# Performance work log

Hardware: AMD Instinct MI355X
Metric: run time of the kernel (lower is better)

The kernel has to match this reference:

```python
import jax, jax.numpy as jnp
import numpy as np

H, DH = 16, 32  # hardcoded by E's shape [16, seq, 32]


def setup_inputs() -> dict:
    key = jax.random.key(0)
    k1, k2 = jax.random.split(key)
    B, S = 2, 2048
    x = jax.random.normal(k1, (B, S, 3 * H * DH), dtype=jnp.float32)
    E = jax.random.normal(k2, (H, S, DH), dtype=jnp.float32) * 0.02  # learned rel-pos table
    return {"x": x, "E": E}


def _skew(rel):
    # Music-Transformer skew trick: rel [B,H,S,S] -> relative-position alignment.
    B, Hh, S, _ = rel.shape
    rel = jnp.pad(rel, ((0, 0), (0, 0), (0, 0), (1, 0)))  # pad left on last dim
    rel = rel.reshape(B, Hh, S + 1, S)[:, :, 1:]
    return rel


def reference(x, E):
    B, S, _ = x.shape
    q, k, v = jnp.split(x, 3, axis=2)

    def heads(t):
        return t.reshape(B, S, H, DH).transpose(0, 2, 1, 3)  # [B,H,S,DH]

    q, k, v = heads(q), heads(k), heads(v)
    present = jnp.stack([k, v], axis=1)  # [B,2,H,S,DH]

    w = jnp.einsum('bhsd,bhtd->bhst', q, k)            # content scores
    rel = _skew(jnp.einsum('bhsd,hmd->bhsm', q, E))    # relative-position scores
    w = (w + rel) * jax.lax.rsqrt(jnp.float32(DH))     # scale AFTER adding rel (as in source)

    i = jnp.arange(S)[:, None]
    j = jnp.arange(S)[None, :]
    b = (i >= j).astype(w.dtype)                       # causal mask (nd == ns)
    w = w * b - jnp.float32(1e10) * (1.0 - b)
    w = jax.nn.softmax(w, axis=-1)

    a = jnp.einsum('bhst,bhtd->bhsd', w, v)
    a = a.transpose(0, 2, 1, 3).reshape(B, S, H * DH)  # merge heads -> [B,S,512]
    return a, present
```

## Files before the change

kernel.cpp:

```cpp
#include <hip/hip_runtime.h>
#include <hip/hip_bf16.h>

#define NH   16
#define DHD  32
#define SEQ  2048
#define NB   2
#define XROW 1536
#define PP   72

typedef unsigned short u16;
typedef __attribute__((ext_vector_type(8))) short bf16x8;
typedef __attribute__((ext_vector_type(4))) float f32x4;

static __device__ __forceinline__ u16 f2b(float f) {
    __hip_bfloat16 h = __float2bfloat16(f);
    return *(u16*)&h;
}

__global__ __launch_bounds__(256)
void prep_all(const float* __restrict__ x, const float* __restrict__ E,
              u16* __restrict__ Kb, u16* __restrict__ Vt, u16* __restrict__ Eb) {
    __shared__ float t[64][33];
    int bid = blockIdx.x;
    int tid = threadIdx.x;
    if (bid < 1024) {
        long o = ((long)bid * 256 + tid) * 8;
        int d = (int)(o & 31);
        int s = (int)((o >> 5) & (SEQ - 1));
        int bh = (int)(o >> 16);
        int b = bh >> 4, h = bh & 15;
        const float* src = x + ((long)(b * SEQ + s)) * XROW + 512 + h * 32 + d;
        float4 f0 = *(const float4*)src, f1 = *(const float4*)(src + 4);
        u16 pk[8] = {f2b(f0.x), f2b(f0.y), f2b(f0.z), f2b(f0.w),
                     f2b(f1.x), f2b(f1.y), f2b(f1.z), f2b(f1.w)};
        *(uint4*)(Kb + o) = *(uint4*)pk;
    } else if (bid < 1536) {
        long o = ((long)(bid - 1024) * 256 + tid) * 8;
        const float* src = E + o;
        float4 f0 = *(const float4*)src, f1 = *(const float4*)(src + 4);
        u16 pk[8] = {f2b(f0.x), f2b(f0.y), f2b(f0.z), f2b(f0.w),
                     f2b(f1.x), f2b(f1.y), f2b(f1.z), f2b(f1.w)};
        *(uint4*)(Eb + o) = *(uint4*)pk;
    } else {
        int vb = bid - 1536;
        int bh = vb & 31;
        int s0 = (vb >> 5) << 6;
        int b = bh >> 4, h = bh & 15;
        int sr = tid >> 3, d4 = (tid & 7) * 4;
        const float* base = x + (long)b * SEQ * XROW + 1024 + h * 32;
        float4 f = *(const float4*)(base + (long)(s0 + sr) * XROW + d4);
        t[sr][d4] = f.x; t[sr][d4+1] = f.y; t[sr][d4+2] = f.z; t[sr][d4+3] = f.w;
        f = *(const float4*)(base + (long)(s0 + sr + 32) * XROW + d4);
        t[sr+32][d4] = f.x; t[sr+32][d4+1] = f.y; t[sr+32][d4+2] = f.z; t[sr+32][d4+3] = f.w;
        __syncthreads();
        int d = tid >> 3, sg = (tid & 7) * 8;
        u16 pk[8];
#pragma unroll
        for (int k = 0; k < 8; ++k) pk[k] = f2b(t[sg + k][d]);
        *(uint4*)(Vt + ((long)(bh * 32 + d)) * SEQ + s0 + sg) = *(uint4*)pk;
    }
}

__global__ __launch_bounds__(256, 8)
void attn_mfma(const float* __restrict__ x, const u16* __restrict__ Kb,
               const u16* __restrict__ Vt, const u16* __restrict__ Eb,
               float* __restrict__ out, float* __restrict__ pres) {
    __shared__ u16  pls[4][16 * PP];
    __shared__ float comb[4][16][33];

    int bh = blockIdx.x & 31;
    int gt = 127 - (blockIdx.x >> 5);
    int b = bh >> 4, h = bh & 15;
    int wv   = threadIdx.x >> 6;
    int lane = threadIdx.x & 63;
    int n16  = lane & 15;
    int quad = lane >> 4;
    int i0 = gt * 16;

    const u16* Kbh = Kb + (long)bh * SEQ * 32;
    const u16* Vbh = Vt + (long)bh * 32 * SEQ;
    const u16* Ebh = Eb + (long)h * SEQ * 32;

    const float scale = 0.17677669529663687f;
    bf16x8 qf;
    {
        const float* qp = x + ((long)(b * SEQ) + i0 + n16) * XROW + h * 32 + quad * 8;
        float4 f0 = *(const float4*)qp, f1 = *(const float4*)(qp + 4);
        u16 pk[8] = {f2b(f0.x*scale), f2b(f0.y*scale), f2b(f0.z*scale), f2b(f0.w*scale),
                     f2b(f1.x*scale), f2b(f1.y*scale), f2b(f1.z*scale), f2b(f1.w*scale)};
        qf = *(bf16x8*)pk;
    }

    bf16x8 ones;
#pragma unroll
    for (int k = 0; k < 8; ++k) ones[k] = (short)0x3F80;

    f32x4 O0 = {0.f,0.f,0.f,0.f}, O1 = {0.f,0.f,0.f,0.f}, Os = {0.f,0.f,0.f,0.f};
    const f32x4 zero = {0.f,0.f,0.f,0.f};

    u16* pw = &pls[wv][0];
    int cbase = 15 - quad * 4 + n16;
    int permhi = (lane & 48) << 2;

    int nch = (i0 >> 6) + 1;
    for (int ch = wv; ch < nch; ch += 4) {
        int j0c = ch << 6;
        int mw0 = 2032 - i0 + j0c;

        f32x4 P0, P1;
        float rel0[4];
        {
            int row = mw0 + n16; if (row > SEQ - 1) row = SEQ - 1;
            bf16x8 ef = *(const bf16x8*)(Ebh + (long)row * 32 + quad * 8);
            P0 = __builtin_amdgcn_mfma_f32_16x16x32_bf16(qf, ef, zero, 0, 0, 0);
        }
#pragma unroll
        for (int r = 0; r < 4; ++r) {
            int addr = permhi | (((cbase - r) & 15) << 2);
            rel0[r] = __int_as_float(
                __builtin_amdgcn_ds_bpermute(addr, __float_as_int(P0[r])));
        }
        f32x4 w[4];
#pragma unroll
        for (int s = 0; s < 4; ++s) {
            {
                int row = mw0 + 16 * (s + 1) + n16; if (row > SEQ - 1) row = SEQ - 1;
                bf16x8 ef = *(const bf16x8*)(Ebh + (long)row * 32 + quad * 8);
                P1 = __builtin_amdgcn_mfma_f32_16x16x32_bf16(qf, ef, zero, 0, 0, 0);
            }
            f32x4 C;
            {
                bf16x8 kf = *(const bf16x8*)(Kbh + (long)(j0c + 16*s + n16) * 32 + quad * 8);
                C = __builtin_amdgcn_mfma_f32_16x16x32_bf16(qf, kf, zero, 0, 0, 0);
            }
#pragma unroll
            for (int r = 0; r < 4; ++r) {
                int c = cbase - r;
                int addr = permhi | ((c & 15) << 2);
                float rel1 = __int_as_float(
                    __builtin_amdgcn_ds_bpermute(addr, __float_as_int(P1[r])));
                float rel = (c < 16) ? rel0[r] : rel1;
                w[s][r] = C[r] + rel;
                rel0[r] = rel1;
            }
            P0 = P1;
        }

        if (ch == nch - 1) {
            int jb = j0c + n16 - i0;
#pragma unroll
            for (int s = 0; s < 4; ++s)
#pragma unroll
                for (int r = 0; r < 4; ++r)
                    if (jb + 16 * s > quad * 4 + r) w[s][r] = -1e30f;
        }

#pragma unroll
        for (int s = 0; s < 4; ++s)
#pragma unroll
            for (int r = 0; r < 4; ++r)
                w[s][r] = __expf(w[s][r]);

#pragma unroll
        for (int s = 0; s < 4; ++s)
#pragma unroll
            for (int r = 0; r < 4; ++r)
                pw[(quad * 4 + r) * PP + 16 * s + n16] = f2b(w[s][r]);

        bf16x8 pa0 = *(const bf16x8*)(pw + n16 * PP + quad * 8);
        bf16x8 pa1 = *(const bf16x8*)(pw + n16 * PP + 32 + quad * 8);

        bf16x8 v00 = *(const bf16x8*)(Vbh + (long)n16 * SEQ        + j0c      + quad * 8);
        bf16x8 v01 = *(const bf16x8*)(Vbh + (long)n16 * SEQ        + j0c + 32 + quad * 8);
        bf16x8 v10 = *(const bf16x8*)(Vbh + (long)(16 + n16) * SEQ + j0c      + quad * 8);
        bf16x8 v11 = *(const bf16x8*)(Vbh + (long)(16 + n16) * SEQ + j0c + 32 + quad * 8);

        O0 = __builtin_amdgcn_mfma_f32_16x16x32_bf16(pa0, v00, O0, 0, 0, 0);
        O0 = __builtin_amdgcn_mfma_f32_16x16x32_bf16(pa1, v01, O0, 0, 0, 0);
        O1 = __builtin_amdgcn_mfma_f32_16x16x32_bf16(pa0, v10, O1, 0, 0, 0);
        O1 = __builtin_amdgcn_mfma_f32_16x16x32_bf16(pa1, v11, O1, 0, 0, 0);
        Os = __builtin_amdgcn_mfma_f32_16x16x32_bf16(pa0, ones, Os, 0, 0, 0);
        Os = __builtin_amdgcn_mfma_f32_16x16x32_bf16(pa1, ones, Os, 0, 0, 0);
    }

#pragma unroll
    for (int r = 0; r < 4; ++r) {
        comb[wv][quad * 4 + r][n16]      = O0[r];
        comb[wv][quad * 4 + r][16 + n16] = O1[r];
        if (n16 == 0) comb[wv][quad * 4 + r][32] = Os[r];
    }
    __syncthreads();

    int row = threadIdx.x >> 4;
    int c2  = (threadIdx.x & 15) * 2;
    float s0 = 0.f, s1 = 0.f, ls = 0.f;
#pragma unroll
    for (int v = 0; v < 4; ++v) {
        s0 += comb[v][row][c2];
        s1 += comb[v][row][c2 + 1];
        ls += comb[v][row][32];
    }
    float inv = 1.0f / ls;
    float* op = out + ((long)(b * SEQ) + i0 + row) * 512 + h * 32 + c2;
    op[0] = s0 * inv;
    op[1] = s1 * inv;

    {
        long o = ((long)blockIdx.x * 256 + threadIdx.x) * 4;
        int d0 = (int)(o & 31);
        int s  = (int)((o >> 5) & (SEQ - 1));
        int hh = (int)((o >> 16) & (NH - 1));
        int cc = (int)((o >> 20) & 1);
        int bb = (int)(o >> 21);
        const float4* in = (const float4*)(x + ((long)(bb * SEQ + s)) * XROW
                                           + (1 + cc) * 512 + hh * 32 + d0);
        *((float4*)(pres + o)) = in[0];
    }
}

__global__ void present_copy(const float* __restrict__ x, float* __restrict__ pres) {
    long o = ((long)blockIdx.x * blockDim.x + threadIdx.x) * 4;
    int d0 = (int)(o & 31);
    int s  = (int)((o >> 5) & (SEQ - 1));
    int h  = (int)((o >> 16) & (NH - 1));
    int c  = (int)((o >> 20) & 1);
    int b  = (int)(o >> 21);
    const float4* in = (const float4*)(x + ((long)(b * SEQ + s)) * XROW
                                       + (1 + c) * 512 + h * 32 + d0);
    *((float4*)(pres + o)) = in[0];
}

__global__ __launch_bounds__(128)
void attn_mono(const float* __restrict__ x, const float* __restrict__ E,
               float* __restrict__ out) {
    __shared__ float kt[64][36];
    __shared__ float vt[64][36];
    __shared__ float et[192][33];
    int bh = blockIdx.x & 31;
    int rt = 15 - (blockIdx.x >> 5);
    int b = bh >> 4, h = bh & 15;
    int tid = threadIdx.x;
    int r0 = rt * 128;
    int i = r0 + tid;
    float q[DHD];
    const float4* q4 = (const float4*)(x + ((long)(b * SEQ + i)) * XROW + h * 32);
#pragma unroll
    for (int t = 0; t < 8; ++t) ((float4*)q)[t] = q4[t];
    float m = -1e30f, l = 0.f;
    float acc[DHD];
#pragma unroll
    for (int d = 0; d < DHD; ++d) acc[d] = 0.f;
    const float* Eh = E + (long)h * SEQ * DHD;
    int ntile = (rt + 1) * 2;
    for (int t0 = 0; t0 < ntile; ++t0) {
        int j0 = t0 * 64;
        {
            int r = tid & 63, isv = tid >> 6;
            const float4* s4 = (const float4*)(x + ((long)(b * SEQ + j0 + r)) * XROW
                                               + (1 + isv) * 512 + h * 32);
            float4 tmp[8];
#pragma unroll
            for (int t = 0; t < 8; ++t) tmp[t] = s4[t];
            float* dst = isv ? &vt[r][0] : &kt[r][0];
#pragma unroll
            for (int t = 0; t < 8; ++t) ((float4*)dst)[t] = tmp[t];
        }
        {
            int eb0 = (SEQ - 1) - (r0 + 127) + j0;
#pragma unroll
            for (int p = 0; p < 12; ++p) {
                int idx = p * 128 + tid;
                int r = idx >> 3, qq = idx & 7;
                int gr = eb0 + r; if (gr > SEQ - 1) gr = SEQ - 1;
                float4 gg = *(const float4*)(Eh + (long)gr * DHD + qq * 4);
                et[r][qq*4+0] = gg.x; et[r][qq*4+1] = gg.y;
                et[r][qq*4+2] = gg.z; et[r][qq*4+3] = gg.w;
            }
        }
        __syncthreads();
        int jend = i - j0 + 1; if (jend > 64) jend = 64;
        int er0 = 127 - tid;
        for (int jj = 0; jj < jend; ++jj) {
            const float* ep = &et[er0 + jj][0];
            float dk = 0.f, de = 0.f;
#pragma unroll
            for (int d = 0; d < DHD; ++d) {
                dk = __builtin_fmaf(q[d], kt[jj][d], dk);
                de = __builtin_fmaf(q[d], ep[d], de);
            }
            float sc = (dk + de) * 0.17677669529663687f;
            if (sc > m) {
                float r = __expf(m - sc);
                l *= r;
#pragma unroll
                for (int d = 0; d < DHD; ++d) acc[d] *= r;
                m = sc;
            }
            float p = __expf(sc - m);
            l += p;
#pragma unroll
            for (int d = 0; d < DHD; ++d)
                acc[d] = __builtin_fmaf(p, vt[jj][d], acc[d]);
        }
        __syncthreads();
    }
    float inv = 1.0f / l;
    float* op = out + ((long)(b * SEQ + i)) * 512 + h * 32;
#pragma unroll
    for (int t = 0; t < 8; ++t) {
        float4 w;
        w.x = acc[t*4+0]*inv; w.y = acc[t*4+1]*inv;
        w.z = acc[t*4+2]*inv; w.w = acc[t*4+3]*inv;
        ((float4*)op)[t] = w;
    }
}

extern "C" void kernel_launch(void* const* d_in, const int* in_sizes, int n_in,
                              void* d_out, int out_size, void* d_ws, size_t ws_size,
                              hipStream_t stream) {
    const float* x = (const float*)d_in[0];
    const float* E = (const float*)d_in[1];
    if (n_in >= 2 && in_sizes[0] == 1048576) { const float* t = x; x = E; E = t; }
    float* a    = (float*)d_out;
    float* pres = a + (long)NB * SEQ * NH * DHD;

    const long KN = (long)NB * NH * SEQ * 32;
    const long EN = (long)NH * SEQ * 32;
    const size_t WS_NEED = (size_t)(2 * KN + EN) * sizeof(u16);
    if (ws_size >= WS_NEED) {
        u16* Kb = (u16*)d_ws;
        u16* Vt = Kb + KN;
        u16* Eb = Vt + KN;
        prep_all<<<dim3(2560), dim3(256), 0, stream>>>(x, E, Kb, Vt, Eb);
        attn_mfma<<<dim3(4096), dim3(256), 0, stream>>>(x, Kb, Vt, Eb, a, pres);
    } else {
        attn_mono<<<dim3(512), dim3(128), 0, stream>>>(x, E, a);
        present_copy<<<dim3(4096), dim3(256), 0, stream>>>(x, pres);
    }
}
```

Before: 149.7 us.

## Pair causal query tiles per block to balance work and halve grid

New measurement: 167.5 us. 1.12x slower.

```diff
diff --git a/kernel.cpp b/kernel.cpp
--- a/kernel.cpp
+++ b/kernel.cpp
@@ -15,6 +15,11 @@
 static __device__ __forceinline__ u16 f2b(float f) {
     __hip_bfloat16 h = __float2bfloat16(f);
     return *(u16*)&h;
+}
+static __device__ __forceinline__ u16 f2b_fast(float f) {
+    unsigned u = __float_as_uint(f);
+    u += 0x7FFFu + ((u >> 16) & 1u);
+    return (u16)(u >> 16);
 }
 
 __global__ __launch_bounds__(256)
@@ -69,152 +74,164 @@
     __shared__ float comb[4][16][33];
 
     int bh = blockIdx.x & 31;
-    int gt = 127 - (blockIdx.x >> 5);
+    int pr = blockIdx.x >> 5;
     int b = bh >> 4, h = bh & 15;
     int wv   = threadIdx.x >> 6;
     int lane = threadIdx.x & 63;
     int n16  = lane & 15;
     int quad = lane >> 4;
-    int i0 = gt * 16;
 
     const u16* Kbh = Kb + (long)bh * SEQ * 32;
     const u16* Vbh = Vt + (long)bh * 32 * SEQ;
     const u16* Ebh = Eb + (long)h * SEQ * 32;
 
+    bf16x8 ones;
+#pragma unroll
+    for (int k = 0; k < 8; ++k) ones[k] = (short)0x3F80;
+
+    const f32x4 zero = {0.f,0.f,0.f,0.f};
     const float scale = 0.17677669529663687f;
-    bf16x8 qf;
-    {
-        const float* qp = x + ((long)(b * SEQ) + i0 + n16) * XROW + h * 32 + quad * 8;
-        float4 f0 = *(const float4*)qp, f1 = *(const float4*)(qp + 4);
-        u16 pk[8] = {f2b(f0.x*scale), f2b(f0.y*scale), f2b(f0.z*scale), f2b(f0.w*scale),
-                     f2b(f1.x*scale), f2b(f1.y*scale), f2b(f1.z*scale), f2b(f1.w*scale)};
-        qf = *(bf16x8*)pk;
-    }
-
-    bf16x8 ones;
-#pragma unroll
-    for (int k = 0; k < 8; ++k) ones[k] = (short)0x3F80;
-
-    f32x4 O0 = {0.f,0.f,0.f,0.f}, O1 = {0.f,0.f,0.f,0.f}, Os = {0.f,0.f,0.f,0.f};
-    const f32x4 zero = {0.f,0.f,0.f,0.f};
-
     u16* pw = &pls[wv][0];
     int cbase = 15 - quad * 4 + n16;
     int permhi = (lane & 48) << 2;
 
-    int nch = (i0 >> 6) + 1;
-    for (int ch = wv; ch < nch; ch += 4) {
-        int j0c = ch << 6;
-        int mw0 = 2032 - i0 + j0c;
-
-        f32x4 P0, P1;
-        float rel0[4];
+    for (int half = 0; half < 2; ++half) {
+        int gt = half ? (127 - pr) : pr;
+        int i0 = gt * 16;
+
+        bf16x8 qf;
         {
-            int row = mw0 + n16; if (row > SEQ - 1) row = SEQ - 1;
-            bf16x8 ef = *(const bf16x8*)(Ebh + (long)row * 32 + quad * 8);
-            P0 = __builtin_amdgcn_mfma_f32_16x16x32_bf16(qf, ef, zero, 0, 0, 0);
-        }
+            const float* qp = x + ((long)(b * SEQ) + i0 + n16) * XROW + h * 32 + quad * 8;
+            float4 f0 = *(const float4*)qp, f1 = *(const float4*)(qp + 4);
+            u16 pk[8] = {f2b_fast(f0.x*scale), f2b_fast(f0.y*scale),
+                         f2b_fast(f0.z*scale), f2b_fast(f0.w*scale),
+                         f2b_fast(f1.x*scale), f2b_fast(f1.y*scale),
+                         f2b_fast(f1.z*scale), f2b_fast(f1.w*scale)};
+            qf = *(bf16x8*)pk;
+        }
+
+        f32x4 O0 = {0.f,0.f,0.f,0.f}, O1 = {0.f,0.f,0.f,0.f}, Os = {0.f,0.f,0.f,0.f};
+
+        int nch = (i0 >> 6) + 1;
+        for (int ch = wv; ch < nch; ch += 4) {
+            int j0c = ch << 6;
+            int mw0 = 2032 - i0 + j0c;
+
+            f32x4 P0, P1;
+            float rel0[4];
+            {
+                int row = mw0 + n16; if (row > SEQ - 1) row = SEQ - 1;
+                bf16x8 ef = *(const bf16x8*)(Ebh + (long)row * 32 + quad * 8);
+                P0 = __builtin_amdgcn_mfma_f32_16x16x32_bf16(qf, ef, zero, 0, 0, 0);
+            }
+#pragma unroll
+            for (int r = 0; r < 4; ++r) {
+                int addr = permhi | (((cbase - r) & 15) << 2);
+                rel0[r] = __int_as_float(
+                    __builtin_amdgcn_ds_bpermute(addr, __float_as_int(P0[r])));
+            }
+            f32x4 w[4];
+#pragma unroll
+            for (int s = 0; s < 4; ++s) {
+                {
+                    int row = mw0 + 16 * (s + 1) + n16; if (row > SEQ - 1) row = SEQ - 1;
+                    bf16x8 ef = *(const bf16x8*)(Ebh + (long)row * 32 + quad * 8);
+                    P1 = __builtin_amdgcn_mfma_f32_16x16x32_bf16(qf, ef, zero, 0, 0, 0);
+                }
+                f32x4 C;
+                {
+                    bf16x8 kf = *(const bf16x8*)(Kbh + (long)(j0c + 16*s + n16) * 32 + quad * 8);
+                    C = __builtin_amdgcn_mfma_f32_16x16x32_bf16(qf, kf, zero, 0, 0, 0);
+                }
+#pragma unroll
+                for (int r = 0; r < 4; ++r) {
+                    int c = cbase - r;
+                    int addr = permhi | ((c & 15) << 2);
+                    float rel1 = __int_as_float(
+                        __builtin_amdgcn_ds_bpermute(addr, __float_as_int(P1[r])));
+                    float rel = (c < 16) ? rel0[r] : rel1;
+                    w[s][r] = C[r] + rel;
+                    rel0[r] = rel1;
+                }
+                P0 = P1;
+            }
+
+            if (ch == nch - 1) {
+                int jb = j0c + n16 - i0;
+#pragma unroll
+                for (int s = 0; s < 4; ++s)
+#pragma unroll
+                    for (int r = 0; r < 4; ++r)
+                        if (jb + 16 * s > quad * 4 + r) w[s][r] = -1e30f;
+            }
+
+#pragma unroll
+            for (int s = 0; s < 4; ++s)
+#pragma unroll
+                for (int r = 0; r < 4; ++r)
+                    w[s][r] = __expf(w[s][r]);
+
+#pragma unroll
+            for (int s = 0; s < 4; ++s)
+#pragma unroll
+                for (int r = 0; r < 4; ++r)
+                    pw[(quad * 4 + r) * PP + 16 * s + n16] = f2b_fast(w[s][r]);
+
+            bf16x8 pa0 = *(const bf16x8*)(pw + n16 * PP + quad * 8);
+            bf16x8 pa1 = *(const bf16x8*)(pw + n16 * PP + 32 + quad * 8);
+
+            bf16x8 v00 = *(const bf16x8*)(Vbh + (long)n16 * SEQ        + j0c      + quad * 8);
+            bf16x8 v01 = *(const bf16x8*)(Vbh + (long)n16 * SEQ        + j0c + 32 + quad * 8);
+            bf16x8 v10 = *(const bf16x8*)(Vbh + (long)(16 + n16) * SEQ + j0c      + quad * 8);
+            bf16x8 v11 = *(const bf16x8*)(Vbh + (long)(16 + n16) * SEQ + j0c + 32 + quad * 8);
+
+            O0 = __builtin_amdgcn_mfma_f32_16x16x32_bf16(pa0, v00, O0, 0, 0, 0);
+            O0 = __builtin_amdgcn_mfma_f32_16x16x32_bf16(pa1, v01, O0, 0, 0, 0);
+            O1 = __builtin_amdgcn_mfma_f32_16x16x32_bf16(pa0, v10, O1, 0, 0, 0);
+            O1 = __builtin_amdgcn_mfma_f32_16x16x32_bf16(pa1, v11, O1, 0, 0, 0);
+            Os = __builtin_amdgcn_mfma_f32_16x16x32_bf16(pa0, ones, Os, 0, 0, 0);
+            Os = __builtin_amdgcn_mfma_f32_16x16x32_bf16(pa1, ones, Os, 0, 0, 0);
+        }
+
+        if (half) __syncthreads();
+
 #pragma unroll
         for (int r = 0; r < 4; ++r) {
-            int addr = permhi | (((cbase - r) & 15) << 2);
-            rel0[r] = __int_as_float(
-                __builtin_amdgcn_ds_bpermute(addr, __float_as_int(P0[r])));
-        }
-        f32x4 w[4];
-#pragma unroll
-        for (int s = 0; s < 4; ++s) {
-            {
-                int row = mw0 + 16 * (s + 1) + n16; if (row > SEQ - 1) row = SEQ - 1;
-                bf16x8 ef = *(const bf16x8*)(Ebh + (long)row * 32 + quad * 8);
-                P1 = __builtin_amdgcn_mfma_f32_16x16x32_bf16(qf, ef, zero, 0, 0, 0);
-            }
-            f32x4 C;
-            {
-                bf16x8 kf = *(const bf16x8*)(Kbh + (long)(j0c + 16*s + n16) * 32 + quad * 8);
-                C = __builtin_amdgcn_mfma_f32_16x16x32_bf16(qf, kf, zero, 0, 0, 0);
-            }
-#pragma unroll
-            for (int r = 0; r < 4; ++r) {
-                int c = cbase - r;
-                int addr = permhi | ((c & 15) << 2);
-                float rel1 = __int_as_float(
-                    __builtin_amdgcn_ds_bpermute(addr, __float_as_int(P1[r])));
-                float rel = (c < 16) ? rel0[r] : rel1;
-                w[s][r] = C[r] + rel;
-                rel0[r] = rel1;
-            }
-            P0 = P1;
-        }
-
-        if (ch == nch - 1) {
-            int jb = j0c + n16 - i0;
-#pragma unroll
-            for (int s = 0; s < 4; ++s)
-#pragma unroll
-                for (int r = 0; r < 4; ++r)
-                    if (jb + 16 * s > quad * 4 + r) w[s][r] = -1e30f;
-        }
-
-#pragma unroll
-        for (int s = 0; s < 4; ++s)
-#pragma unroll
-            for (int r = 0; r < 4; ++r)
-                w[s][r] = __expf(w[s][r]);
-
-#pragma unroll
-        for (int s = 0; s < 4; ++s)
-#pragma unroll
-            for (int r = 0; r < 4; ++r)
-                pw[(quad * 4 + r) * PP + 16 * s + n16] = f2b(w[s][r]);
-
-        bf16x8 pa0 = *(const bf16x8*)(pw + n16 * PP + quad * 8);
-        bf16x8 pa1 = *(const bf16x8*)(pw + n16 * PP + 32 + quad * 8);
-
-        bf16x8 v00 = *(const bf16x8*)(Vbh + (long)n16 * SEQ        + j0c      + quad * 8);
-        bf16x8 v01 = *(const bf16x8*)(Vbh + (long)n16 * SEQ        + j0c + 32 + quad * 8);
-        bf16x8 v10 = *(const bf16x8*)(Vbh + (long)(16 + n16) * SEQ + j0c      + quad * 8);
-        bf16x8 v11 = *(const bf16x8*)(Vbh + (long)(16 + n16) * SEQ + j0c + 32 + quad * 8);
-
-        O0 = __builtin_amdgcn_mfma_f32_16x16x32_bf16(pa0, v00, O0, 0, 0, 0);
-        O0 = __builtin_amdgcn_mfma_f32_16x16x32_bf16(pa1, v01, O0, 0, 0, 0);
-        O1 = __builtin_amdgcn_mfma_f32_16x16x32_bf16(pa0, v10, O1, 0, 0, 0);
-        O1 = __builtin_amdgcn_mfma_f32_16x16x32_bf16(pa1, v11, O1, 0, 0, 0);
-        Os = __builtin_amdgcn_mfma_f32_16x16x32_bf16(pa0, ones, Os, 0, 0, 0);
-        Os = __builtin_amdgcn_mfma_f32_16x16x32_bf16(pa1, ones, Os, 0, 0, 0);
-    }
-
-#pragma unroll
-    for (int r = 0; r < 4; ++r) {
-        comb[wv][quad * 4 + r][n16]      = O0[r];
-        comb[wv][quad * 4 + r][16 + n16] = O1[r];
-        if (n16 == 0) comb[wv][quad * 4 + r][32] = Os[r];
-    }
-    __syncthreads();
-
-    int row = threadIdx.x >> 4;
-    int c2  = (threadIdx.x & 15) * 2;
-    float s0 = 0.f, s1 = 0.f, ls = 0.f;
-#pragma unroll
-    for (int v = 0; v < 4; ++v) {
-        s0 += comb[v][row][c2];
-        s1 += comb[v][row][c2 + 1];
-        ls += comb[v][row][32];
-    }
-    float inv = 1.0f / ls;
-    float* op = out + ((long)(b * SEQ) + i0 + row) * 512 + h * 32 + c2;
-    op[0] = s0 * inv;
-    op[1] = s1 * inv;
+            comb[wv][quad * 4 + r][n16]      = O0[r];
+            comb[wv][quad * 4 + r][16 + n16] = O1[r];
+            if (n16 == 0) comb[wv][quad * 4 + r][32] = Os[r];
+        }
+        __syncthreads();
+
+        int row = threadIdx.x >> 4;
+        int c2  = (threadIdx.x & 15) * 2;
+        float s0 = 0.f, s1 = 0.f, ls = 0.f;
+#pragma unroll
+        for (int v = 0; v < 4; ++v) {
+            s0 += comb[v][row][c2];
+            s1 += comb[v][row][c2 + 1];
+            ls += comb[v][row][32];
+        }
+        float inv = 1.0f / ls;
+        float* op = out + ((long)(b * SEQ) + i0 + row) * 512 + h * 32 + c2;
+        op[0] = s0 * inv;
+        op[1] = s1 * inv;
+    }
 
     {
-        long o = ((long)blockIdx.x * 256 + threadIdx.x) * 4;
-        int d0 = (int)(o & 31);
-        int s  = (int)((o >> 5) & (SEQ - 1));
-        int hh = (int)((o >> 16) & (NH - 1));
-        int cc = (int)((o >> 20) & 1);
-        int bb = (int)(o >> 21);
-        const float4* in = (const float4*)(x + ((long)(bb * SEQ + s)) * XROW
-                                           + (1 + cc) * 512 + hh * 32 + d0);
-        *((float4*)(pres + o)) = in[0];
+        long o = ((long)blockIdx.x * 256 + threadIdx.x) * 8;
+#pragma unroll
+        for (int t = 0; t < 2; ++t) {
+            long oo = o + t * 4;
+            int d0 = (int)(oo & 31);
+            int s  = (int)((oo >> 5) & (SEQ - 1));
+            int hh = (int)((oo >> 16) & (NH - 1));
+            int cc = (int)((oo >> 20) & 1);
+            int bb = (int)(oo >> 21);
+            const float4* in = (const float4*)(x + ((long)(bb * SEQ + s)) * XROW
+                                               + (1 + cc) * 512 + hh * 32 + d0);
+            *((float4*)(pres + oo)) = in[0];
+        }
     }
 }
 
@@ -332,7 +349,7 @@
         u16* Vt = Kb + KN;
         u16* Eb = Vt + KN;
         prep_all<<<dim3(2560), dim3(256), 0, stream>>>(x, E, Kb, Vt, Eb);
-        attn_mfma<<<dim3(4096), dim3(256), 0, stream>>>(x, Kb, Vt, Eb, a, pres);
+        attn_mfma<<<dim3(2048), dim3(256), 0, stream>>>(x, Kb, Vt, Eb, a, pres);
     } else {
         attn_mono<<<dim3(512), dim3(128), 0, stream>>>(x, E, a);
         present_copy<<<dim3(4096), dim3(256), 0, stream>>>(x, pres);
```
